# Optimization experiments

Measured on AMD Instinct MI355X. Metric: run time of the kernel, lower is better.

The kernel has to match this reference:

```python
import jax, jax.numpy as jnp
import numpy as np

VOCAB = 100000
EMBED = 300
BATCH = 131072
NEG = 10


def setup_inputs() -> dict:
    key = jax.random.key(0)
    k1, k2, k3, k4, k5 = jax.random.split(key, 5)
    center_words = jax.random.randint(k1, (BATCH,), 0, VOCAB)
    context_words = jax.random.randint(k2, (BATCH,), 0, VOCAB)
    neg_samples = jax.random.randint(k3, (BATCH, NEG), 0, VOCAB)
    in_embed = jax.random.normal(k4, (VOCAB, EMBED), dtype=jnp.float32)
    out_embed = jax.random.normal(k5, (VOCAB, EMBED), dtype=jnp.float32)
    return {
        "center_words": center_words,
        "context_words": context_words,
        "neg_samples": neg_samples,
        "in_embed": in_embed,
        "out_embed": out_embed,
    }


def reference(center_words, context_words, neg_samples, in_embed, out_embed):
    center_e = in_embed[center_words]          # [B, D]
    context_e = out_embed[context_words]       # [B, D]
    neg_e = out_embed[neg_samples]             # [B, K, D]
    pos_scores = jnp.sum(center_e * context_e, axis=1)            # [B]
    neg_scores = jnp.einsum("bkd,bd->bk", neg_e, center_e)        # [B, K]
    pos_loss = jax.nn.log_sigmoid(pos_scores)                      # [B]
    neg_loss = jnp.sum(jax.nn.log_sigmoid(-neg_scores), axis=1)   # [B]
    return -jnp.mean(pos_loss + neg_loss)
```

## Files before the change

kernel.cpp:

```cpp
#include <hip/hip_runtime.h>
#include <math.h>

#define VOCABN 100000
#define EMBED 300
#define BATCH 131072
#define NEG 10
#define PD 3

typedef float float2v __attribute__((ext_vector_type(2)));


template <bool HI>
__device__ __forceinline__ float2v cvt2(unsigned int w) {
    return __builtin_amdgcn_cvt_pk_f32_fp8((int)w, HI);
}
template <bool HI>
__device__ __forceinline__ unsigned int pk2(unsigned int old, float a, float b) {
    return (unsigned int)__builtin_amdgcn_cvt_pk_fp8_f32(a, b, (int)old, HI);
}

__device__ __forceinline__ float2v dq8p(const float2v* c, uint4 q, float2v acc) {
    acc += c[0] * cvt2<false>(q.x);
    acc += c[1] * cvt2<true >(q.x);
    acc += c[2] * cvt2<false>(q.y);
    acc += c[3] * cvt2<true >(q.y);
    acc += c[4] * cvt2<false>(q.z);
    acc += c[5] * cvt2<true >(q.z);
    acc += c[6] * cvt2<false>(q.w);
    acc += c[7] * cvt2<true >(q.w);
    return acc;
}

__device__ __forceinline__ void unp8p(uint4 q, float2v* f) {
    f[0] = cvt2<false>(q.x);
    f[1] = cvt2<true >(q.x);
    f[2] = cvt2<false>(q.y);
    f[3] = cvt2<true >(q.y);
    f[4] = cvt2<false>(q.z);
    f[5] = cvt2<true >(q.z);
    f[6] = cvt2<false>(q.w);
    f[7] = cvt2<true >(q.w);
}


template <int N>
__device__ __forceinline__ float dpps(float x) {
    int s = __builtin_amdgcn_update_dpp(0, __float_as_int(x), 0x110 | N, 0xF, 0xF, true);
    return x + __int_as_float(s);
}
__device__ __forceinline__ float reduce16d(float v) {
    v = dpps<1>(v);
    v = dpps<2>(v);
    v = dpps<4>(v);
    v = dpps<8>(v);
    return v;
}


__device__ __forceinline__ float dot4(const float4 a, const float4 b) {
    return a.x * b.x + a.y * b.y + a.z * b.z + a.w * b.w;
}

__device__ __forceinline__ float lsig(float x) {
    float ax = fabsf(x);
    return fminf(x, 0.0f) - __logf(1.0f + __expf(-ax));
}

__device__ __forceinline__ float reduce16(float v) {
    v += __shfl_xor(v, 1);
    v += __shfl_xor(v, 2);
    v += __shfl_xor(v, 4);
    v += __shfl_xor(v, 8);
    return v;
}

__global__ void sgns_zero_acc(double* acc) { *acc = 0.0; }

__global__ void sgns_finalize(const double* __restrict__ acc, float* __restrict__ out) {
    *out = (float)(-(*acc) / (double)BATCH);
}


__global__ __launch_bounds__(256) void cvt_fp8s(const float* __restrict__ src,
                                                uint4* __restrict__ mainT,
                                                uint4* __restrict__ tailT, int nrows) {
    const int total = nrows * 20;
    const int stride = gridDim.x * blockDim.x;
    for (int i = blockIdx.x * blockDim.x + threadIdx.x; i < total; i += stride) {
        const int r = i / 20;
        const int q = i - r * 20;
        if (q < 16) {
            const float4* s = reinterpret_cast<const float4*>(src + (size_t)r * EMBED + q * 16);
            float4 a = s[0], b = s[1], c = s[2], d = s[3];
            uint4 o;
            unsigned int w;
            w = pk2<false>(0, a.x, a.y); o.x = pk2<true>(w, a.z, a.w);
            w = pk2<false>(0, b.x, b.y); o.y = pk2<true>(w, b.z, b.w);
            w = pk2<false>(0, c.x, c.y); o.z = pk2<true>(w, c.z, c.w);
            w = pk2<false>(0, d.x, d.y); o.w = pk2<true>(w, d.z, d.w);
            mainT[(size_t)r * 16 + q] = o;
        } else {
            const int t = q - 16;
            uint4 o = make_uint4(0u, 0u, 0u, 0u);
            if (t < 3) {
                const float4* s = reinterpret_cast<const float4*>(src + (size_t)r * EMBED + 256 + t * 16);
                float4 a = s[0], b = s[1], c = s[2];
                float4 d = make_float4(0.f, 0.f, 0.f, 0.f);
                if (t < 2) d = s[3];
                unsigned int w;
                w = pk2<false>(0, a.x, a.y); o.x = pk2<true>(w, a.z, a.w);
                w = pk2<false>(0, b.x, b.y); o.y = pk2<true>(w, b.z, b.w);
                w = pk2<false>(0, c.x, c.y); o.z = pk2<true>(w, c.z, c.w);
                w = pk2<false>(0, d.x, d.y); o.w = pk2<true>(w, d.z, d.w);
            }
            tailT[(size_t)r * 4 + t] = o;
        }
    }
}


__global__ __launch_bounds__(256) void sgns_fp8(
    const int* __restrict__ center_words,
    const int* __restrict__ context_words,
    const int* __restrict__ neg_samples,
    const uint4* __restrict__ inM,  const uint4* __restrict__ inT,
    const uint4* __restrict__ outM, const uint4* __restrict__ outT,
    double* __restrict__ acc)
{
    const int lane = threadIdx.x & 15;
    const int group = (blockIdx.x * blockDim.x + threadIdx.x) >> 4;
    const int nGroups = (gridDim.x * blockDim.x) >> 4;
    const int tl = (lane < 3) ? lane : 0;
    const float tmask = (lane < 3) ? 1.0f : 0.0f;

    float tsum = 0.0f;

    for (int b = group; b < BATCH; b += nGroups) {
        const int cw = center_words[b];
        const int xw = context_words[b];
        const int2* np = reinterpret_cast<const int2*>(neg_samples + (size_t)b * NEG);
        int2 q0 = np[0], q1 = np[1], q2 = np[2], q3 = np[3], q4 = np[4];
        int idx[11] = {xw, q0.x, q0.y, q1.x, q1.y, q2.x, q2.y, q3.x, q3.y, q4.x, q4.y};

        uint4 cm = inM[(size_t)cw * 16 + lane];
        uint4 ct = inT[(size_t)cw * 4 + tl];
        float2v cf2[16];
        unp8p(cm, cf2);
        unp8p(ct, cf2 + 8);
        #pragma unroll
        for (int j = 8; j < 16; ++j) cf2[j] *= tmask;

        float part[11];
        uint4 bm[PD], bt[PD];
        #pragma unroll
        for (int j = 0; j < PD - 1; ++j) {
            bm[j] = outM[(size_t)idx[j] * 16 + lane];
            bt[j] = outT[(size_t)idx[j] * 4 + tl];
        }
        #pragma unroll
        for (int j = 0; j < 11; ++j) {
            if (j + PD - 1 < 11) {
                bm[(j + PD - 1) % PD] = outM[(size_t)idx[j + PD - 1] * 16 + lane];
                bt[(j + PD - 1) % PD] = outT[(size_t)idx[j + PD - 1] * 4 + tl];
            }
            float2v a2 = dq8p(cf2, bm[j % PD], (float2v){0.f, 0.f});
            a2 = dq8p(cf2 + 8, bt[j % PD], a2);
            part[j] = a2.x + a2.y;
        }

        #pragma unroll
        for (int j = 0; j < 11; ++j) part[j] = reduce16d(part[j]);

        float loss = lsig(part[0]);
        #pragma unroll
        for (int j = 1; j < 11; ++j) loss += lsig(-part[j]);

        tsum += (lane == 15) ? loss : 0.0f;
    }

    float w = tsum;
    #pragma unroll
    for (int m = 1; m < 64; m <<= 1) w += __shfl_xor(w, m);

    __shared__ double ssum[4];
    const int wid = threadIdx.x >> 6;
    if ((threadIdx.x & 63) == 0) ssum[wid] = (double)w;
    __syncthreads();
    if (threadIdx.x == 0) {
        atomicAdd(acc, ssum[0] + ssum[1] + ssum[2] + ssum[3]);
    }
}


__global__ __launch_bounds__(256) void sgns_f32(
    const int* __restrict__ center_words,
    const int* __restrict__ context_words,
    const int* __restrict__ neg_samples,
    const float* __restrict__ in_embed,
    const float* __restrict__ out_embed,
    double* __restrict__ acc)
{
    const int lane = threadIdx.x & 15;
    const int group = (blockIdx.x * blockDim.x + threadIdx.x) >> 4;
    const int nGroups = (gridDim.x * blockDim.x) >> 4;

    const float4* inE = reinterpret_cast<const float4*>(in_embed);
    const float4* outE = reinterpret_cast<const float4*>(out_embed);
    const int RU = EMBED / 4;
    const int TAIL = RU - 64;

    float tsum = 0.0f;

    for (int b = group; b < BATCH; b += nGroups) {
        const int c = center_words[b];
        const int ctx = context_words[b];

        const float4* crow = inE + (size_t)c * RU;
        float4 c0 = crow[lane + 0];
        float4 c1 = crow[lane + 16];
        float4 c2 = crow[lane + 32];
        float4 c3 = crow[lane + 48];
        float4 c4 = make_float4(0.f, 0.f, 0.f, 0.f);
        if (lane < TAIL) c4 = crow[lane + 64];

        const float4* xrow = outE + (size_t)ctx * RU;
        float p = dot4(c0, xrow[lane + 0])
                + dot4(c1, xrow[lane + 16])
                + dot4(c2, xrow[lane + 32])
                + dot4(c3, xrow[lane + 48]);
        if (lane < TAIL) p += dot4(c4, xrow[lane + 64]);
        p = reduce16(p);

        float loss = lsig(p);

        #pragma unroll
        for (int k = 0; k < NEG; ++k) {
            const int nk = neg_samples[b * NEG + k];
            const float4* nrow = outE + (size_t)nk * RU;
            float s = dot4(c0, nrow[lane + 0])
                    + dot4(c1, nrow[lane + 16])
                    + dot4(c2, nrow[lane + 32])
                    + dot4(c3, nrow[lane + 48]);
            if (lane < TAIL) s += dot4(c4, nrow[lane + 64]);
            s = reduce16(s);
            loss += lsig(-s);
        }

        tsum += (lane == 0) ? loss : 0.0f;
    }

    float w = tsum;
    #pragma unroll
    for (int m = 1; m < 64; m <<= 1) w += __shfl_xor(w, m);

    __shared__ double ssum[4];
    const int wid = threadIdx.x >> 6;
    if ((threadIdx.x & 63) == 0) ssum[wid] = (double)w;
    __syncthreads();
    if (threadIdx.x == 0) {
        atomicAdd(acc, ssum[0] + ssum[1] + ssum[2] + ssum[3]);
    }
}


extern "C" void kernel_launch(void* const* d_in, const int* in_sizes, int n_in,
                              void* d_out, int out_size, void* d_ws, size_t ws_size,
                              hipStream_t stream) {
    const int* center = (const int*)d_in[0];
    const int* context = (const int*)d_in[1];
    const int* negs = (const int*)d_in[2];
    const float* inE = (const float*)d_in[3];
    const float* outE = (const float*)d_in[4];
    float* out = (float*)d_out;
    double* acc = (double*)d_ws;

    sgns_zero_acc<<<1, 1, 0, stream>>>(acc);

    const size_t MAIN_B = (size_t)VOCABN * 16 * 16;
    const size_t TAIL_B = (size_t)VOCABN * 4 * 16;
    const size_t need = 256 + 2 * (MAIN_B + TAIL_B);

    if (ws_size >= need) {
        char* base = (char*)d_ws + 256;
        uint4* inM  = (uint4*)(base);
        uint4* inT  = (uint4*)(base + MAIN_B);
        uint4* outM = (uint4*)(base + MAIN_B + TAIL_B);
        uint4* outT = (uint4*)(base + 2 * MAIN_B + TAIL_B);
        cvt_fp8s<<<4096, 256, 0, stream>>>(inE, inM, inT, VOCABN);
        cvt_fp8s<<<4096, 256, 0, stream>>>(outE, outM, outT, VOCABN);
        sgns_fp8<<<2048, 256, 0, stream>>>(center, context, negs,
                                           inM, inT, outM, outT, acc);
    } else {
        sgns_f32<<<2048, 256, 0, stream>>>(center, context, negs, inE, outE, acc);
    }

    sgns_finalize<<<1, 1, 0, stream>>>(acc, out);
}
```

Measured before the change: 151.2 us.

## Stage fp8 embedding row gathers through LDS with async global_load_lds pipeline

Replaces the register-prefetched gathers of center and negative/context rows with direct global-to-LDS loads (global_load_lds). A 4-slot ring buffer per wavefront is refilled three rows ahead, and completion is tracked with explicit vmcnt waits. The goal is deeper memory-level parallelism without the register pressure of holding prefetched rows. The cost is extra LDS traffic and footprint, and it relies on hand-counted vmcnt values that must match the number of outstanding loads.

```diff
diff --git a/kernel.cpp b/kernel.cpp
--- a/kernel.cpp
+++ b/kernel.cpp
@@ -5,7 +5,6 @@
 #define EMBED 300
 #define BATCH 131072
 #define NEG 10
-#define PD 3
 
 typedef float float2v __attribute__((ext_vector_type(2)));
 
@@ -54,6 +53,23 @@
     v = dpps<4>(v);
     v = dpps<8>(v);
     return v;
+}
+
+
+template <int N>
+__device__ __forceinline__ void waitv() {
+    asm volatile("s_waitcnt vmcnt(%0)" :: "n"(N) : "memory");
+}
+
+__device__ __forceinline__ void gl16(const void* g, void* l) {
+    __builtin_amdgcn_global_load_lds(
+        (const __attribute__((address_space(1))) void*)g,
+        (__attribute__((address_space(3))) void*)l, 16, 0, 0);
+}
+__device__ __forceinline__ void gl4(const void* g, void* l) {
+    __builtin_amdgcn_global_load_lds(
+        (const __attribute__((address_space(1))) void*)g,
+        (__attribute__((address_space(3))) void*)l, 4, 0, 0);
 }
 
 
@@ -127,11 +143,26 @@
     const uint4* __restrict__ outM, const uint4* __restrict__ outT,
     double* __restrict__ acc)
 {
-    const int lane = threadIdx.x & 15;
-    const int group = (blockIdx.x * blockDim.x + threadIdx.x) >> 4;
+    __shared__ uint4 LB4[(4 * 6400) / 16];
+    unsigned char* lds0 = (unsigned char*)LB4;
+
+    const int tid = threadIdx.x;
+    const int lane15 = tid & 15;
+    const int lane63 = tid & 63;
+    const int gw = (tid >> 4) & 3;
+    unsigned char* wb = lds0 + (tid >> 6) * 6400;
+
+    const int group = (blockIdx.x * blockDim.x + tid) >> 4;
     const int nGroups = (gridDim.x * blockDim.x) >> 4;
-    const int tl = (lane < 3) ? lane : 0;
-    const float tmask = (lane < 3) ? 1.0f : 0.0f;
+    const int tl = (lane15 < 3) ? lane15 : 0;
+    const float tmask = (lane15 < 3) ? 1.0f : 0.0f;
+
+    const char* inMb  = (const char*)inM;
+    const char* inTb  = (const char*)inT;
+    const char* outMb = (const char*)outM;
+    const char* outTb = (const char*)outT;
+    const int goffM = lane15 << 4;
+    const int goffT = lane15 << 2;
 
     float tsum = 0.0f;
 
@@ -142,8 +173,17 @@
         int2 q0 = np[0], q1 = np[1], q2 = np[2], q3 = np[3], q4 = np[4];
         int idx[11] = {xw, q0.x, q0.y, q1.x, q1.y, q2.x, q2.y, q3.x, q3.y, q4.x, q4.y};
 
-        uint4 cm = inM[(size_t)cw * 16 + lane];
-        uint4 ct = inT[(size_t)cw * 4 + tl];
+        gl16(inMb + ((size_t)cw << 8) + goffM, wb + 5120);
+        gl4 (inTb + ((size_t)cw << 6) + goffT, wb + 6144);
+        #pragma unroll
+        for (int j = 0; j < 3; ++j) {
+            gl16(outMb + ((size_t)idx[j] << 8) + goffM, wb + j * 1280);
+            gl4 (outTb + ((size_t)idx[j] << 6) + goffT, wb + j * 1280 + 1024);
+        }
+
+        waitv<6>();
+        uint4 cm = *reinterpret_cast<const uint4*>(wb + 5120 + lane63 * 16);
+        uint4 ct = *reinterpret_cast<const uint4*>(wb + 6144 + gw * 64 + tl * 16);
         float2v cf2[16];
         unp8p(cm, cf2);
         unp8p(ct, cf2 + 8);
@@ -151,22 +191,27 @@
         for (int j = 8; j < 16; ++j) cf2[j] *= tmask;
 
         float part[11];
-        uint4 bm[PD], bt[PD];
-        #pragma unroll
-        for (int j = 0; j < PD - 1; ++j) {
-            bm[j] = outM[(size_t)idx[j] * 16 + lane];
-            bt[j] = outT[(size_t)idx[j] * 4 + tl];
+
+#define ROW_STEP(J, W)                                                                     \
+        {                                                                                  \
+            if ((J) + 3 < 11) {                                                            \
+                const int rr = idx[(J) + 3];                                               \
+                const int ss = ((J) + 3) & 3;                                              \
+                gl16(outMb + ((size_t)rr << 8) + goffM, wb + ss * 1280);                   \
+                gl4 (outTb + ((size_t)rr << 6) + goffT, wb + ss * 1280 + 1024);            \
+            }                                                                              \
+            waitv<W>();                                                                    \
+            uint4 bmv = *reinterpret_cast<const uint4*>(wb + ((J) & 3) * 1280 + lane63 * 16);             \
+            uint4 btv = *reinterpret_cast<const uint4*>(wb + ((J) & 3) * 1280 + 1024 + gw * 64 + tl * 16);\
+            float2v a2 = dq8p(cf2, bmv, (float2v){0.f, 0.f});                              \
+            a2 = dq8p(cf2 + 8, btv, a2);                                                   \
+            part[(J)] = a2.x + a2.y;                                                       \
         }
-        #pragma unroll
-        for (int j = 0; j < 11; ++j) {
-            if (j + PD - 1 < 11) {
-                bm[(j + PD - 1) % PD] = outM[(size_t)idx[j + PD - 1] * 16 + lane];
-                bt[(j + PD - 1) % PD] = outT[(size_t)idx[j + PD - 1] * 4 + tl];
-            }
-            float2v a2 = dq8p(cf2, bm[j % PD], (float2v){0.f, 0.f});
-            a2 = dq8p(cf2 + 8, bt[j % PD], a2);
-            part[j] = a2.x + a2.y;
-        }
+
+        ROW_STEP(0, 6) ROW_STEP(1, 6) ROW_STEP(2, 6) ROW_STEP(3, 6)
+        ROW_STEP(4, 6) ROW_STEP(5, 6) ROW_STEP(6, 6) ROW_STEP(7, 6)
+        ROW_STEP(8, 4) ROW_STEP(9, 2) ROW_STEP(10, 0)
+#undef ROW_STEP
 
         #pragma unroll
         for (int j = 0; j < 11; ++j) part[j] = reduce16d(part[j]);
@@ -175,7 +220,7 @@
         #pragma unroll
         for (int j = 1; j < 11; ++j) loss += lsig(-part[j]);
 
-        tsum += (lane == 15) ? loss : 0.0f;
+        tsum += (lane15 == 15) ? loss : 0.0f;
     }
 
     float w = tsum;
@@ -183,10 +228,10 @@
     for (int m = 1; m < 64; m <<= 1) w += __shfl_xor(w, m);
 
     __shared__ double ssum[4];
-    const int wid = threadIdx.x >> 6;
-    if ((threadIdx.x & 63) == 0) ssum[wid] = (double)w;
+    const int wid = tid >> 6;
+    if (lane63 == 0) ssum[wid] = (double)w;
     __syncthreads();
-    if (threadIdx.x == 0) {
+    if (tid == 0) {
         atomicAdd(acc, ssum[0] + ssum[1] + ssum[2] + ssum[3]);
     }
 }
```

Measured after the change: 157.3 us. 4.0% more time.
